# Kernel tuning notes

Hardware: AMD Instinct MI355X
Metric: run time of the kernel (lower is better)

## Reference

```python
import jax, jax.numpy as jnp
import numpy as np

B, L, H, C, A = 8, 4096, 512, 64, 512
NEG = -1000000000.0

def setup_inputs() -> dict:
    key = jax.random.key(0)
    ks = jax.random.split(key, 6)
    hidden_states = jax.random.normal(ks[0], (B, L, H), dtype=jnp.float32)
    critical_mask = jax.random.randint(ks[1], (B, L, 1), 0, 2).astype(bool)
    count_active_channels = jax.random.randint(ks[2], (B, L, 1), 0, 64).astype(jnp.int32)
    channel_activity = jax.random.normal(ks[3], (B, L, C), dtype=jnp.float32)
    proj_w = jax.random.normal(ks[4], (H, A), dtype=jnp.float32) * 0.02
    proj_b = jnp.zeros((A,), dtype=jnp.float32)
    score_w = jax.random.normal(ks[5], (A, 1), dtype=jnp.float32) * 0.02
    score_b = jnp.zeros((1,), dtype=jnp.float32)
    return {"hidden_states": hidden_states, "critical_mask": critical_mask,
            "count_active_channels": count_active_channels,
            "channel_activity": channel_activity,
            "proj_w": proj_w, "proj_b": proj_b,
            "score_w": score_w, "score_b": score_b}

def reference(hidden_states, critical_mask, count_active_channels, channel_activity,
              proj_w, proj_b, score_w, score_b):
    mask = critical_mask[..., 0].astype(bool)                       # (B,L)
    count_signal = count_active_channels[..., 0].astype(hidden_states.dtype)  # (B,L)
    activity = jnp.maximum(channel_activity.astype(hidden_states.dtype), 0.0)  # (B,L,C)
    # score(tanh(proj(h)))  -> (B,L)
    logits = (jnp.tanh(hidden_states @ proj_w + proj_b) @ score_w + score_b)[..., 0]
    logits = logits + jnp.log1p(jnp.maximum(count_signal, 0.0))
    channel_mask = activity > 0                                      # (B,L,C)
    # (B,C,L) masked logits with log1p activity bias
    channel_logits = logits[:, None, :] + jnp.log1p(jnp.swapaxes(activity, 1, 2))
    channel_logits = jnp.where(jnp.swapaxes(channel_mask, 1, 2), channel_logits, NEG)
    has_channel_any = channel_mask.any(axis=1)                       # (B,C)
    weights = jax.nn.softmax(channel_logits, axis=-1)                # (B,C,L)
    weights = jnp.where(has_channel_any[..., None], weights, 0.0)
    channel_contexts = jnp.einsum('bcl,blh->bch', weights, hidden_states)  # (B,C,H)
    fallback = jnp.broadcast_to(hidden_states[:, -1:, :], channel_contexts.shape)
    channel_contexts = jnp.where(has_channel_any[..., None], channel_contexts, fallback)
    mix = activity / jnp.maximum(activity.sum(axis=2, keepdims=True), 1.0)  # (B,L,C)
    expanded_context = jnp.einsum('blc,bch->blh', mix, channel_contexts)    # (B,L,H)
    max_count = jnp.maximum(count_signal.max(axis=1, keepdims=True), 1.0)
    density_gate = 1.0 + count_signal / max_count                    # (B,L)
    attended = jnp.where(mask[..., None], expanded_context * density_gate[..., None], hidden_states)
    return attended, weights
```

## Files before the change

kernel.cpp:

```cpp
#include <hip/hip_runtime.h>
#include <hip/hip_bf16.h>
#include <math.h>

#define NEGV (-1000000000.0f)
constexpr int Bb = 8, Ll = 4096, Hh = 512, Cc = 64, Aa = 512;

typedef float f32x4 __attribute__((ext_vector_type(4)));
typedef short s16x8 __attribute__((ext_vector_type(8)));

__device__ inline ushort f2bf(float f) {
  union { float f; uint u; } v; v.f = f;
  uint u = v.u;
  return (ushort)((u + 0x7FFFu + ((u >> 16) & 1u)) >> 16);
}

__device__ inline uint bfpack2(float x, float y) {
  __hip_bfloat162 h = __float22bfloat162_rn(make_float2(x, y));
  union { __hip_bfloat162 h; uint u; } v; v.h = h;
  return v.u;
}

__device__ __forceinline__ void gl16(const void* g, void* l) {
  __builtin_amdgcn_global_load_lds(
      reinterpret_cast<const __attribute__((address_space(1))) unsigned int*>(
          reinterpret_cast<uintptr_t>(g)),
      reinterpret_cast<__attribute__((address_space(3))) unsigned int*>(
          reinterpret_cast<uintptr_t>(l)),
      16, 0, 0);
}

__global__ void k_cvt(const float* __restrict__ hid, ushort* __restrict__ hidb) {
  size_t i = (size_t)blockIdx.x * 256 + threadIdx.x;
#pragma unroll
  for (int r = 0; r < 4; ++r, i += 524288) {
    const float4* p = (const float4*)(hid + i * 8);
    float4 x = p[0], y = p[1];
    uint4 u = {bfpack2(x.x, x.y), bfpack2(x.z, x.w),
               bfpack2(y.x, y.y), bfpack2(y.z, y.w)};
    *(uint4*)(hidb + i * 8) = u;
  }
}

__global__ void k_init(const int* __restrict__ cnt, const float* __restrict__ sb,
                       float* __restrict__ logits, int* __restrict__ cmax) {
  int i = blockIdx.x * 256 + threadIdx.x;
  int c = cnt[i];
  logits[i] = sb[0] + log1pf(fmaxf((float)c, 0.f));
  int m = c;
#pragma unroll
  for (int s = 32; s; s >>= 1) m = max(m, __shfl_xor(m, s));
  if ((threadIdx.x & 63) == 0) atomicMax(&cmax[i >> 12], m);
}

__global__ void kT_pw(const float* __restrict__ pw, ushort* __restrict__ pwT) {
  __shared__ ushort s[64][65];
  const int k0 = (blockIdx.x >> 3) * 64, a0 = (blockIdx.x & 7) * 64;
  const int t = threadIdx.x;
#pragma unroll
  for (int i = 0; i < 16; ++i) {
    int e = t + i * 256;
    int kk = e >> 6, aa = e & 63;
    s[aa][kk] = f2bf(pw[(size_t)(k0 + kk) * Aa + a0 + aa]);
  }
  __syncthreads();
#pragma unroll
  for (int i = 0; i < 16; ++i) {
    int e = t + i * 256;
    int aa = e >> 6, kk = e & 63;
    pwT[(size_t)(a0 + aa) * Hh + k0 + kk] = s[aa][kk];
  }
}

__global__ __launch_bounds__(256) void k0_gemm(
    const ushort* __restrict__ hidb, const ushort* __restrict__ pwT,
    const float* __restrict__ pb, const float* __restrict__ sw,
    float* __restrict__ logits) {
  __shared__ ushort smem[16384];
  const int bm = blockIdx.x, bn = blockIdx.y;
  const int tid = threadIdx.x;
  const int lane = tid & 63;
  const int w = tid >> 6;
  const int wm = w >> 1, wn = w & 1;
  const int lc = lane & 15, lq = lane >> 4;

  const int srow = tid >> 2;
  const int schunk = (tid & 3) * 8;
  const ushort* Ag = hidb + ((size_t)(bm * 128 + srow)) * Hh + schunk;
  const ushort* Bg = pwT + ((size_t)(bn * 128 + srow)) * Hh + schunk;
  const int wrow = 16 * w;

  f32x4 acc[4][4];
#pragma unroll
  for (int mi = 0; mi < 4; ++mi)
#pragma unroll
    for (int ni = 0; ni < 4; ++ni) acc[mi][ni] = (f32x4){0.f, 0.f, 0.f, 0.f};

  const int aoffc = (wm * 64 + lc) * 32 + lq * 8;
  const int boffc = (wn * 64 + lc) * 32 + lq * 8;

#define K0_STAGE(buf, kb)                                   \
  do {                                                      \
    const ushort* ag = Ag + (kb) * 32;                      \
    const ushort* bg = Bg + (kb) * 32;                      \
    ushort* la = smem + (buf) * 4096 + wrow * 32;           \
    ushort* lb = smem + 8192 + (buf) * 4096 + wrow * 32;    \
    gl16(ag, la);                                           \
    gl16(ag + 64 * Hh, la + 64 * 32);                       \
    gl16(bg, lb);                                           \
    gl16(bg + 64 * Hh, lb + 64 * 32);                       \
  } while (0)

  K0_STAGE(0, 0);
  __syncthreads();

  int buf = 0;
  for (int kb = 0; kb < 16; ++kb) {
    if (kb < 15) K0_STAGE(buf ^ 1, kb + 1);
    const ushort* Ab = smem + buf * 4096;
    const ushort* Bt = smem + 8192 + buf * 4096;
    s16x8 af[4], bfr[4];
#pragma unroll
    for (int mi = 0; mi < 4; ++mi)
      af[mi] = *(const s16x8*)(Ab + aoffc + mi * 512);
#pragma unroll
    for (int ni = 0; ni < 4; ++ni)
      bfr[ni] = *(const s16x8*)(Bt + boffc + ni * 512);
#pragma unroll
    for (int mi = 0; mi < 4; ++mi)
#pragma unroll
      for (int ni = 0; ni < 4; ++ni)
        acc[mi][ni] = __builtin_amdgcn_mfma_f32_16x16x32_bf16(
            af[mi], bfr[ni], acc[mi][ni], 0, 0, 0);
    __syncthreads();
    buf ^= 1;
  }
#undef K0_STAGE

  float pbv[4], swv[4];
#pragma unroll
  for (int ni = 0; ni < 4; ++ni) {
    int n = bn * 128 + wn * 64 + ni * 16 + lc;
    pbv[ni] = pb[n];
    swv[ni] = sw[n];
  }
#pragma unroll
  for (int mi = 0; mi < 4; ++mi) {
#pragma unroll
    for (int r = 0; r < 4; ++r) {
      float s = 0.f;
#pragma unroll
      for (int ni = 0; ni < 4; ++ni) {
        float x = acc[mi][ni][r] + pbv[ni];
        float e = __expf(2.f * x);
        float th = 1.f - 2.f / (e + 1.f);
        s = fmaf(th, swv[ni], s);
      }
      s += __shfl_xor(s, 1);
      s += __shfl_xor(s, 2);
      s += __shfl_xor(s, 4);
      s += __shfl_xor(s, 8);
      if (lc == 0) {
        int m = bm * 128 + wm * 64 + mi * 16 + lq * 4 + r;
        atomicAdd(&logits[m], s);
      }
    }
  }
}

__global__ void k2_transpose(const float* __restrict__ act,
                             float* __restrict__ actT,
                             float* __restrict__ dinv) {
  __shared__ float t64[64][65];
  const int b = blockIdx.x >> 6;
  const int l0 = (blockIdx.x & 63) * 64;
  const int tid = threadIdx.x;
#pragma unroll
  for (int i = 0; i < 16; ++i) {
    int e = tid + i * 256;
    int l = e >> 6, c = e & 63;
    float v = act[((size_t)(b * Ll + l0 + l)) * Cc + c];
    t64[l][c] = fmaxf(v, 0.f);
  }
  __syncthreads();
  if (tid < 64) {
    float s = 0.f;
#pragma unroll 8
    for (int c = 0; c < 64; ++c) s += t64[tid][c];
    dinv[b * Ll + l0 + tid] = 1.0f / fmaxf(s, 1.0f);
  }
#pragma unroll
  for (int i = 0; i < 16; ++i) {
    int e = tid + i * 256;
    int c = e >> 6, lq = e & 63;
    actT[((size_t)(b * Cc + c)) * Ll + l0 + lq] = t64[lq][c];
  }
}

__global__ void k3_softmax(const float* __restrict__ actT,
                           const float* __restrict__ logits,
                           float* __restrict__ wout,
                           ushort* __restrict__ wb16,
                           int* __restrict__ hasany) {
  __shared__ float rmax[4], rcnt[4], rsum[4];
  const int bid = blockIdx.x;
  const int b = bid >> 6;
  const int tid = threadIdx.x;
  const float* arow = actT + (size_t)bid * Ll;

  float xs[16];
  float lmax = NEGV, fcnt = 0.f;
#pragma unroll
  for (int i = 0; i < 16; ++i) {
    int l = tid + i * 256;
    float a = arow[l];
    float x;
    if (a > 0.f) {
      x = logits[b * Ll + l] + log1pf(a);
      fcnt += 1.f;
    } else {
      x = NEGV;
    }
    xs[i] = x;
    lmax = fmaxf(lmax, x);
  }
#pragma unroll
  for (int m = 32; m >= 1; m >>= 1) {
    lmax = fmaxf(lmax, __shfl_xor(lmax, m));
    fcnt += __shfl_xor(fcnt, m);
  }
  if ((tid & 63) == 0) { rmax[tid >> 6] = lmax; rcnt[tid >> 6] = fcnt; }
  __syncthreads();
  float m4 = fmaxf(fmaxf(rmax[0], rmax[1]), fmaxf(rmax[2], rmax[3]));
  float call = rcnt[0] + rcnt[1] + rcnt[2] + rcnt[3];

  float lsum = 0.f;
#pragma unroll
  for (int i = 0; i < 16; ++i) {
    float e = expf(xs[i] - m4);
    xs[i] = e;
    lsum += e;
  }
#pragma unroll
  for (int m = 32; m >= 1; m >>= 1) lsum += __shfl_xor(lsum, m);
  if ((tid & 63) == 0) rsum[tid >> 6] = lsum;
  __syncthreads();
  float s = rsum[0] + rsum[1] + rsum[2] + rsum[3];
  int any = call > 0.5f;
  float inv = any ? 1.0f / s : 0.f;
#pragma unroll
  for (int i = 0; i < 16; ++i) {
    float wv = xs[i] * inv;
    wout[(size_t)bid * Ll + tid + i * 256] = wv;
    wb16[(size_t)bid * Ll + tid + i * 256] = f2bf(wv);
  }
  if (tid == 0) hasany[bid] = any;
}

__global__ __launch_bounds__(256) void k5_mfma(
    const ushort* __restrict__ wb16, const float* __restrict__ hid,
    float* __restrict__ pbuf) {
  const int b = blockIdx.x, nt = blockIdx.y, kz = blockIdx.z;
  const int tid = threadIdx.x;
  const int w = tid >> 6, lane = tid & 63;
  const int lc = lane & 15, lq = lane >> 4;
  const int h0 = nt * 128 + w * 32;

  f32x4 acc[4][2];
#pragma unroll
  for (int mi = 0; mi < 4; ++mi)
#pragma unroll
    for (int ni = 0; ni < 2; ++ni) acc[mi][ni] = (f32x4){0.f, 0.f, 0.f, 0.f};

  const ushort* Abase =
      wb16 + (size_t)b * Cc * Ll + (size_t)lc * Ll + kz * 256 + lq * 8;
  const float* Bbase =
      hid + ((size_t)(b * Ll + kz * 256 + lq * 8)) * Hh + h0 + lc;

  for (int kb = 0; kb < 8; ++kb) {
    s16x8 af[4];
#pragma unroll
    for (int mi = 0; mi < 4; ++mi)
      af[mi] = *(const s16x8*)(Abase + (size_t)mi * 16 * Ll + kb * 32);
    s16x8 bf[2];
#pragma unroll
    for (int ni = 0; ni < 2; ++ni) {
      const float* bp = Bbase + (size_t)kb * 32 * Hh + ni * 16;
      uint u0 = bfpack2(bp[0 * Hh], bp[1 * Hh]);
      uint u1 = bfpack2(bp[2 * Hh], bp[3 * Hh]);
      uint u2 = bfpack2(bp[4 * Hh], bp[5 * Hh]);
      uint u3 = bfpack2(bp[6 * Hh], bp[7 * Hh]);
      union { uint4 u4; s16x8 s; } cv;
      cv.u4 = (uint4){u0, u1, u2, u3};
      bf[ni] = cv.s;
    }
#pragma unroll
    for (int mi = 0; mi < 4; ++mi)
#pragma unroll
      for (int ni = 0; ni < 2; ++ni)
        acc[mi][ni] = __builtin_amdgcn_mfma_f32_16x16x32_bf16(
            af[mi], bf[ni], acc[mi][ni], 0, 0, 0);
  }

  const size_t obase = ((size_t)(kz * Bb + b)) * Cc * Hh;
#pragma unroll
  for (int mi = 0; mi < 4; ++mi)
#pragma unroll
    for (int ni = 0; ni < 2; ++ni)
#pragma unroll
      for (int r = 0; r < 4; ++r)
        pbuf[obase + (size_t)(mi * 16 + lq * 4 + r) * Hh + h0 + ni * 16 + lc] =
            acc[mi][ni][r];
}

__global__ void k6_reduce(const float* __restrict__ pbuf,
                          const int* __restrict__ hasany,
                          const float* __restrict__ hid,
                          float* __restrict__ cctx) {
  int idx = blockIdx.x * 256 + threadIdx.x;
  float s = 0.f;
#pragma unroll
  for (int z = 0; z < 16; ++z) s += pbuf[(size_t)z * 262144 + idx];
  int bc = idx >> 9, b = idx >> 15, h = idx & 511;
  cctx[idx] = hasany[bc] ? s : hid[((size_t)(b * Ll + Ll - 1)) * Hh + h];
}

__global__ __launch_bounds__(256, 2) void k7_out(
    const float* __restrict__ hid, const float* __restrict__ act,
    const float* __restrict__ dinv, const float* __restrict__ cctx,
    const int* __restrict__ mask, const int* __restrict__ cnt,
    const int* __restrict__ cmax, float* __restrict__ out) {
  __shared__ float mix[32 * 68];
  __shared__ float gateb[32];
  __shared__ int maskb[32];
  const int b = blockIdx.x;
  const int l0 = blockIdx.y * 32;
  const int tid = threadIdx.x;
  const float maxcf = fmaxf((float)cmax[b], 1.0f);

#pragma unroll
  for (int i = 0; i < 2; ++i) {
    int q = tid + i * 256;
    int t = q >> 4, cq = q & 15;
    float4 a4 = *(const float4*)(act + ((size_t)(b * Ll + l0 + t)) * Cc + cq * 4);
    float dv = dinv[b * Ll + l0 + t];
    a4.x = fmaxf(a4.x, 0.f) * dv;
    a4.y = fmaxf(a4.y, 0.f) * dv;
    a4.z = fmaxf(a4.z, 0.f) * dv;
    a4.w = fmaxf(a4.w, 0.f) * dv;
    *(float4*)(mix + t * 68 + cq * 4) = a4;
  }
  if (tid < 32) {
    int l = l0 + tid;
    maskb[tid] = mask[b * Ll + l];
    gateb[tid] = 1.0f + (float)cnt[b * Ll + l] / maxcf;
  }
  __syncthreads();

  const int tt = tid >> 6;
  const int h = (tid & 63) * 8;
  float acc[8][8];
#pragma unroll
  for (int t = 0; t < 8; ++t)
#pragma unroll
    for (int u = 0; u < 8; ++u) acc[t][u] = 0.f;

#pragma unroll 4
  for (int c = 0; c < 64; ++c) {
    float4 cA = *(const float4*)(cctx + ((size_t)(b * Cc + c)) * Hh + h);
    float4 cB = *(const float4*)(cctx + ((size_t)(b * Cc + c)) * Hh + h + 4);
    float cv[8] = {cA.x, cA.y, cA.z, cA.w, cB.x, cB.y, cB.z, cB.w};
#pragma unroll
    for (int t = 0; t < 8; ++t) {
      float mv = mix[(tt * 8 + t) * 68 + c];
#pragma unroll
      for (int u = 0; u < 8; ++u) acc[t][u] = fmaf(mv, cv[u], acc[t][u]);
    }
  }
#pragma unroll
  for (int t = 0; t < 8; ++t) {
    int tok = tt * 8 + t;
    size_t off = ((size_t)(b * Ll + l0 + tok)) * Hh + h;
    float4 o1, o2;
    if (maskb[tok]) {
      float g = gateb[tok];
      o1 = make_float4(acc[t][0] * g, acc[t][1] * g, acc[t][2] * g, acc[t][3] * g);
      o2 = make_float4(acc[t][4] * g, acc[t][5] * g, acc[t][6] * g, acc[t][7] * g);
    } else {
      o1 = *(const float4*)(hid + off);
      o2 = *(const float4*)(hid + off + 4);
    }
    *(float4*)(out + off) = o1;
    *(float4*)(out + off + 4) = o2;
  }
}

extern "C" void kernel_launch(void* const* d_in, const int* in_sizes, int n_in,
                              void* d_out, int out_size, void* d_ws,
                              size_t ws_size, hipStream_t stream) {
  const float* hid = (const float*)d_in[0];
  const int* mask = (const int*)d_in[1];
  const int* cnt = (const int*)d_in[2];
  const float* act = (const float*)d_in[3];
  const float* pw = (const float*)d_in[4];
  const float* pb = (const float*)d_in[5];
  const float* sw = (const float*)d_in[6];
  const float* sb = (const float*)d_in[7];

  float* out_att = (float*)d_out;
  float* out_w = out_att + (size_t)Bb * Ll * Hh;

  float* ws = (float*)d_ws;
  float* cctx = ws;
  int* cmaxi = (int*)(ws + 262144);
  float* logits = ws + 262152;
  float* actT = ws + 294920;
  float* dinv = ws + 2392072;
  int* hasany = (int*)(ws + 2424840);
  ushort* pwT = (ushort*)(ws + 2425352);
  ushort* wb16 = (ushort*)(ws + 2556424);
  float* pbuf = ws + 3605000;

  ushort* hidb = (ushort*)out_att;

  hipMemsetAsync(cmaxi, 0, 8 * sizeof(int), stream);

  k_cvt<<<2048, 256, 0, stream>>>(hid, hidb);
  k_init<<<128, 256, 0, stream>>>(cnt, sb, logits, cmaxi);
  kT_pw<<<64, 256, 0, stream>>>(pw, pwT);
  k0_gemm<<<dim3(256, 4), 256, 0, stream>>>(hidb, pwT, pb, sw, logits);
  k2_transpose<<<512, 256, 0, stream>>>(act, actT, dinv);
  k3_softmax<<<512, 256, 0, stream>>>(actT, logits, out_w, wb16, hasany);
  k5_mfma<<<dim3(8, 4, 16), 256, 0, stream>>>(wb16, hid, pbuf);
  k6_reduce<<<1024, 256, 0, stream>>>(pbuf, hasany, hid, cctx);
  k7_out<<<dim3(8, 128), 256, 0, stream>>>(hid, act, dinv, cctx, mask, cnt,
                                           cmaxi, out_att);
}
```

Baseline: 276.7 us.

## Reuse bf16 hidden copy in k5 and tile k7 with LDS-staged contexts

k5 now reads the bf16 copy of hidden_states that already exists (stored in the output buffer) instead of loading fp32 values and converting them. This halves the bytes of its B-operand loads and removes the conversion work. k7 is re-tiled to 64 tokens by 128 hidden columns per block, with channel contexts staged into LDS through global_load_lds and the inner loop vectorised over four channels. The tiling adds a grid dimension and drops the two-blocks-per-CU launch bound, which may change occupancy.

```diff
diff --git a/kernel.cpp b/kernel.cpp
--- a/kernel.cpp
+++ b/kernel.cpp
@@ -257,7 +257,7 @@
 }
 
 __global__ __launch_bounds__(256) void k5_mfma(
-    const ushort* __restrict__ wb16, const float* __restrict__ hid,
+    const ushort* __restrict__ wb16, const ushort* __restrict__ hidb,
     float* __restrict__ pbuf) {
   const int b = blockIdx.x, nt = blockIdx.y, kz = blockIdx.z;
   const int tid = threadIdx.x;
@@ -273,32 +273,29 @@
 
   const ushort* Abase =
       wb16 + (size_t)b * Cc * Ll + (size_t)lc * Ll + kz * 256 + lq * 8;
-  const float* Bbase =
-      hid + ((size_t)(b * Ll + kz * 256 + lq * 8)) * Hh + h0 + lc;
+  const ushort* Bbase =
+      hidb + ((size_t)(b * Ll + kz * 256 + lq * 8)) * Hh + h0 + lc;
 
   for (int kb = 0; kb < 8; ++kb) {
     s16x8 af[4];
 #pragma unroll
     for (int mi = 0; mi < 4; ++mi)
       af[mi] = *(const s16x8*)(Abase + (size_t)mi * 16 * Ll + kb * 32);
-    s16x8 bf[2];
+    s16x8 bfv[2];
 #pragma unroll
     for (int ni = 0; ni < 2; ++ni) {
-      const float* bp = Bbase + (size_t)kb * 32 * Hh + ni * 16;
-      uint u0 = bfpack2(bp[0 * Hh], bp[1 * Hh]);
-      uint u1 = bfpack2(bp[2 * Hh], bp[3 * Hh]);
-      uint u2 = bfpack2(bp[4 * Hh], bp[5 * Hh]);
-      uint u3 = bfpack2(bp[6 * Hh], bp[7 * Hh]);
-      union { uint4 u4; s16x8 s; } cv;
-      cv.u4 = (uint4){u0, u1, u2, u3};
-      bf[ni] = cv.s;
+      const ushort* bp = Bbase + (size_t)kb * 32 * Hh + ni * 16;
+      s16x8 t;
+#pragma unroll
+      for (int j = 0; j < 8; ++j) t[j] = (short)bp[(size_t)j * Hh];
+      bfv[ni] = t;
     }
 #pragma unroll
     for (int mi = 0; mi < 4; ++mi)
 #pragma unroll
       for (int ni = 0; ni < 2; ++ni)
         acc[mi][ni] = __builtin_amdgcn_mfma_f32_16x16x32_bf16(
-            af[mi], bf[ni], acc[mi][ni], 0, 0, 0);
+            af[mi], bfv[ni], acc[mi][ni], 0, 0, 0);
   }
 
   const size_t obase = ((size_t)(kz * Bb + b)) * Cc * Hh;
@@ -324,73 +321,83 @@
   cctx[idx] = hasany[bc] ? s : hid[((size_t)(b * Ll + Ll - 1)) * Hh + h];
 }
 
-__global__ __launch_bounds__(256, 2) void k7_out(
+__global__ __launch_bounds__(256) void k7_out(
     const float* __restrict__ hid, const float* __restrict__ act,
     const float* __restrict__ dinv, const float* __restrict__ cctx,
     const int* __restrict__ mask, const int* __restrict__ cnt,
     const int* __restrict__ cmax, float* __restrict__ out) {
-  __shared__ float mix[32 * 68];
-  __shared__ float gateb[32];
-  __shared__ int maskb[32];
+  __shared__ float cct[64][128];
+  __shared__ float mixs[64][64];
+  __shared__ float gateb[64];
+  __shared__ int maskb[64];
   const int b = blockIdx.x;
-  const int l0 = blockIdx.y * 32;
+  const int l0 = blockIdx.y * 64;
+  const int h0 = blockIdx.z * 128;
   const int tid = threadIdx.x;
-  const float maxcf = fmaxf((float)cmax[b], 1.0f);
-
-#pragma unroll
-  for (int i = 0; i < 2; ++i) {
-    int q = tid + i * 256;
-    int t = q >> 4, cq = q & 15;
-    float4 a4 = *(const float4*)(act + ((size_t)(b * Ll + l0 + t)) * Cc + cq * 4);
+  const int w = tid >> 6;
+
+  {
+    const float* g = cctx + (size_t)(b * Cc + (tid >> 5)) * Hh + h0 + (tid & 31) * 4;
+    float* lb = &cct[0][0] + (2 * w) * 128;
+#pragma unroll
+    for (int i = 0; i < 8; ++i)
+      gl16(g + (size_t)(i * 8) * Hh, lb + i * 8 * 128);
+  }
+#pragma unroll
+  for (int i = 0; i < 4; ++i) {
+    int e = tid + i * 256;
+    int t = e >> 4, c4 = (e & 15) * 4;
+    float4 a4 = *(const float4*)(act + ((size_t)(b * Ll + l0 + t)) * Cc + c4);
     float dv = dinv[b * Ll + l0 + t];
     a4.x = fmaxf(a4.x, 0.f) * dv;
     a4.y = fmaxf(a4.y, 0.f) * dv;
     a4.z = fmaxf(a4.z, 0.f) * dv;
     a4.w = fmaxf(a4.w, 0.f) * dv;
-    *(float4*)(mix + t * 68 + cq * 4) = a4;
-  }
-  if (tid < 32) {
+    *(float4*)&mixs[t][c4] = a4;
+  }
+  if (tid < 64) {
     int l = l0 + tid;
     maskb[tid] = mask[b * Ll + l];
-    gateb[tid] = 1.0f + (float)cnt[b * Ll + l] / maxcf;
-  }
-  __syncthreads();
-
-  const int tt = tid >> 6;
-  const int h = (tid & 63) * 8;
-  float acc[8][8];
-#pragma unroll
-  for (int t = 0; t < 8; ++t)
-#pragma unroll
-    for (int u = 0; u < 8; ++u) acc[t][u] = 0.f;
+    gateb[tid] = 1.0f + (float)cnt[b * Ll + l] / fmaxf((float)cmax[b], 1.0f);
+  }
+  __syncthreads();
+
+  const int hcol = (tid & 31) * 4;
+  const int tok0 = (tid >> 5) * 8;
+
+  f32x4 acc[8];
+#pragma unroll
+  for (int t = 0; t < 8; ++t) acc[t] = (f32x4){0.f, 0.f, 0.f, 0.f};
 
 #pragma unroll 4
-  for (int c = 0; c < 64; ++c) {
-    float4 cA = *(const float4*)(cctx + ((size_t)(b * Cc + c)) * Hh + h);
-    float4 cB = *(const float4*)(cctx + ((size_t)(b * Cc + c)) * Hh + h + 4);
-    float cv[8] = {cA.x, cA.y, cA.z, cA.w, cB.x, cB.y, cB.z, cB.w};
+  for (int c0 = 0; c0 < 64; c0 += 4) {
+    f32x4 cv0 = *(const f32x4*)&cct[c0 + 0][hcol];
+    f32x4 cv1 = *(const f32x4*)&cct[c0 + 1][hcol];
+    f32x4 cv2 = *(const f32x4*)&cct[c0 + 2][hcol];
+    f32x4 cv3 = *(const f32x4*)&cct[c0 + 3][hcol];
 #pragma unroll
     for (int t = 0; t < 8; ++t) {
-      float mv = mix[(tt * 8 + t) * 68 + c];
-#pragma unroll
-      for (int u = 0; u < 8; ++u) acc[t][u] = fmaf(mv, cv[u], acc[t][u]);
+      f32x4 mv = *(const f32x4*)&mixs[tok0 + t][c0];
+      f32x4 a = acc[t];
+      a = cv0 * mv.x + a;
+      a = cv1 * mv.y + a;
+      a = cv2 * mv.z + a;
+      a = cv3 * mv.w + a;
+      acc[t] = a;
     }
   }
+
 #pragma unroll
   for (int t = 0; t < 8; ++t) {
-    int tok = tt * 8 + t;
-    size_t off = ((size_t)(b * Ll + l0 + tok)) * Hh + h;
-    float4 o1, o2;
+    int tok = tok0 + t;
+    size_t off = ((size_t)(b * Ll + l0 + tok)) * Hh + h0 + hcol;
+    f32x4 o;
     if (maskb[tok]) {
-      float g = gateb[tok];
-      o1 = make_float4(acc[t][0] * g, acc[t][1] * g, acc[t][2] * g, acc[t][3] * g);
-      o2 = make_float4(acc[t][4] * g, acc[t][5] * g, acc[t][6] * g, acc[t][7] * g);
+      o = acc[t] * gateb[tok];
     } else {
-      o1 = *(const float4*)(hid + off);
-      o2 = *(const float4*)(hid + off + 4);
+      o = *(const f32x4*)(hid + off);
     }
-    *(float4*)(out + off) = o1;
-    *(float4*)(out + off + 4) = o2;
+    *(f32x4*)(out + off) = o;
   }
 }
 
@@ -430,8 +437,8 @@
   k0_gemm<<<dim3(256, 4), 256, 0, stream>>>(hidb, pwT, pb, sw, logits);
   k2_transpose<<<512, 256, 0, stream>>>(act, actT, dinv);
   k3_softmax<<<512, 256, 0, stream>>>(actT, logits, out_w, wb16, hasany);
-  k5_mfma<<<dim3(8, 4, 16), 256, 0, stream>>>(wb16, hid, pbuf);
+  k5_mfma<<<dim3(8, 4, 16), 256, 0, stream>>>(wb16, hidb, pbuf);
   k6_reduce<<<1024, 256, 0, stream>>>(pbuf, hasany, hid, cctx);
-  k7_out<<<dim3(8, 128), 256, 0, stream>>>(hid, act, dinv, cctx, mask, cnt,
-                                           cmaxi, out_att);
-}
+  k7_out<<<dim3(8, 64, 4), 256, 0, stream>>>(hid, act, dinv, cctx, mask, cnt,
+                                             cmaxi, out_att);
+}
```

New measurement: 263.6 us. 1.05x faster.
